# Kernel optimization log

Hardware: AMD Instinct MI355X
Metric: run time of the kernel (lower is better)

Reference implementation:

```python
import jax, jax.numpy as jnp
import numpy as np
import math

NH, NKV, D = 32, 8, 128  # heads, kv heads, head dim

def _alibi_slopes(n):
    cp2 = 2 ** math.floor(math.log2(n))
    base = 2.0 ** (-8.0 / cp2)
    slopes = base ** np.arange(1, cp2 + 1, dtype=np.float32)
    if cp2 != n:
        extra_base = 2.0 ** (-4.0 / cp2)
        extra = extra_base ** np.arange(1, 1 + 2 * (n - cp2), 2, dtype=np.float32)
        slopes = np.concatenate([slopes, extra])
    return slopes.astype(np.float32)

def setup_inputs() -> dict:
    key = jax.random.key(0)
    k1, k2, k3 = jax.random.split(key, 3)
    B, S, H = 4, 1024, 4096
    qkv_out = NH * D + 2 * NKV * D  # 6144
    return {
        "hidden_states": jax.random.normal(k1, (B, S, H), jnp.float32) * 0.02,
        "w_qkv": jax.random.normal(k2, (H, qkv_out), jnp.float32) * 0.02,
        "w_o": jax.random.normal(k3, (NH * D, H), jnp.float32) * 0.02,
    }

def reference(hidden_states, w_qkv, w_o):
    B, S, H = hidden_states.shape
    G = NH // NKV  # query groups per kv head
    scale = D ** -0.5

    qkv = hidden_states @ w_qkv  # [B,S,6144]
    q = qkv[..., : NH * D].reshape(B, S, NKV, G, D)
    k = qkv[..., NH * D : NH * D + NKV * D].reshape(B, S, NKV, D)
    v = qkv[..., NH * D + NKV * D :].reshape(B, S, NKV, D)

    scores = jnp.einsum("bqhgd,bkhd->bhgqk", q, k) * scale  # [B,NKV,G,S,S]

    slopes = jnp.asarray(_alibi_slopes(NH)).reshape(NKV, G)  # head order
    pos = jnp.arange(S)
    rel = pos[:, None] - pos[None, :]  # i - j
    sqrt_dist = jnp.sqrt(jnp.maximum(rel, 0).astype(jnp.float32))
    bias = -slopes[:, :, None, None] * sqrt_dist  # ALiBi-sqrt bias
    bias = jnp.where(rel[None, None] >= 0, bias, -jnp.inf)  # causal mask

    attn = jax.nn.softmax(scores + bias[None], axis=-1)
    out = jnp.einsum("bhgqk,bkhd->bqhgd", attn, v).reshape(B, S, NH * D)
    return out @ w_o
```

## Files before the change

kernel.cpp:

```cpp
#include <hip/hip_runtime.h>
#include <stdint.h>

typedef __attribute__((ext_vector_type(4))) float floatx4;
typedef __attribute__((ext_vector_type(8))) short short8;
typedef unsigned short ushort_t;

#define DEVI __device__ __forceinline__

constexpr int Bc   = 4;
constexpr int Sc   = 1024;
constexpr int Hc   = 4096;
constexpr int NHc  = 32;
constexpr int NKVc = 8;
constexpr int Dc   = 128;
constexpr int QKVO = 6144;
constexpr int Mc   = Bc * Sc;

DEVI ushort_t f2bf(float f) {
  union { float f; unsigned u; } x; x.f = f;
  unsigned u = x.u;
  u += 0x7fffu + ((u >> 16) & 1u);
  return (ushort_t)(u >> 16);
}

DEVI short8 cvt8(floatx4 a, floatx4 b) {
  short8 r;
  r[0] = (short)f2bf(a[0]); r[1] = (short)f2bf(a[1]);
  r[2] = (short)f2bf(a[2]); r[3] = (short)f2bf(a[3]);
  r[4] = (short)f2bf(b[0]); r[5] = (short)f2bf(b[1]);
  r[6] = (short)f2bf(b[2]); r[7] = (short)f2bf(b[3]);
  return r;
}

DEVI void load_lds16(const ushort_t* g, ushort_t* l) {
  __builtin_amdgcn_global_load_lds(
      (const __attribute__((address_space(1))) void*)g,
      (__attribute__((address_space(3))) void*)l, 16, 0, 0);
}

#define BARRIER()  asm volatile("s_barrier" ::: "memory")
#define LGKM0()    asm volatile("s_waitcnt lgkmcnt(0)" ::: "memory")
#define VMCNT(n)   asm volatile("s_waitcnt vmcnt(" #n ")" ::: "memory")

__global__ __launch_bounds__(256)
void cvt_bf16(const float* __restrict__ src, ushort_t* __restrict__ dst, int n8)
{
  const int i = blockIdx.x * 256 + threadIdx.x;
  if (i >= n8) return;
  const floatx4 f0 = *(const floatx4*)(src + (size_t)i * 8);
  const floatx4 f1 = *(const floatx4*)(src + (size_t)i * 8 + 4);
  *(short8*)(dst + (size_t)i * 8) = cvt8(f0, f1);
}

__global__ __launch_bounds__(256)
void transpose_cvt(const float* __restrict__ src, ushort_t* __restrict__ dst,
                   int R, int C)
{
  __shared__ float ts[64][67];
  const int cb = C >> 6;
  const int r0 = (blockIdx.x / cb) << 6;
  const int c0 = (blockIdx.x % cb) << 6;
  const int t  = threadIdx.x;

  const int lr = t >> 4, lc = (t & 15) << 2;
#pragma unroll
  for (int i = 0; i < 4; ++i) {
    const floatx4 v = *(const floatx4*)(src + (size_t)(r0 + lr + 16 * i) * C + c0 + lc);
#pragma unroll
    for (int j = 0; j < 4; ++j) ts[lr + 16 * i][lc + j] = v[j];
  }
  __syncthreads();

  const int c     = ((t >> 6) << 4) + ((t & 63) >> 2);
  const int chunk = t & 3;
  short8 t0, t1;
#pragma unroll
  for (int k = 0; k < 8; ++k) t0[k] = (short)f2bf(ts[chunk * 16 + k][c]);
#pragma unroll
  for (int k = 0; k < 8; ++k) t1[k] = (short)f2bf(ts[chunk * 16 + 8 + k][c]);
  ushort_t* dp = dst + (size_t)(c0 + c) * R + r0 + chunk * 16;
  *(short8*)dp       = t0;
  *(short8*)(dp + 8) = t1;
}

__global__ __launch_bounds__(256)
void v_transpose(const ushort_t* __restrict__ qkv, ushort_t* __restrict__ vt)
{
  __shared__ ushort_t ts[64][72];
  const int bid = blockIdx.x;
  const int db  = bid & 1;
  const int sb  = (bid >> 1) & 15;
  const int hkv = (bid >> 5) & 7;
  const int b   = bid >> 8;
  const int t   = threadIdx.x;

  const ushort_t* src = qkv + (size_t)(b * Sc + sb * 64) * QKVO
                        + (NHc * Dc + NKVc * Dc) + hkv * Dc + db * 64;
  const int lr = t >> 3, lc = (t & 7) * 8;
  *(short8*)&ts[lr][lc]      = *(const short8*)(src + (size_t)lr * QKVO + lc);
  *(short8*)&ts[lr + 32][lc] = *(const short8*)(src + (size_t)(lr + 32) * QKVO + lc);
  __syncthreads();

  ushort_t* dst = vt + ((size_t)(b * NKVc + hkv) * Dc + db * 64) * Sc + sb * 64;
  const int dr  = t >> 2;
  const int sc0 = (t & 3) * 16;
  short8 o0, o1;
#pragma unroll
  for (int k = 0; k < 8; ++k) o0[k] = (short)ts[sc0 + k][dr];
#pragma unroll
  for (int k = 0; k < 8; ++k) o1[k] = (short)ts[sc0 + 8 + k][dr];
  *(short8*)(dst + (size_t)dr * Sc + sc0)     = o0;
  *(short8*)(dst + (size_t)dr * Sc + sc0 + 8) = o1;
}

template<int NFRAG, bool OBF16>
__global__ __launch_bounds__(512, 2)
void gemm_nt8d(const ushort_t* __restrict__ A, const ushort_t* __restrict__ BT,
               void* __restrict__ Cp, int M, int N, int K)
{
  constexpr int BN = 64 * NFRAG;
  __shared__ __align__(16) ushort_t As[2][256 * 64];
  __shared__ __align__(16) ushort_t Bs[2][BN * 64];

  const int nb  = N / BN;
  const int nwg = (M >> 8) * nb;
  int bid = blockIdx.x;
  bid = (bid & 7) * (nwg >> 3) + (bid >> 3);
  const int bm = bid / nb, bn = bid % nb;
  const int m0 = bm << 8, n0 = bn * BN;

  const int tid  = threadIdx.x;
  const int wid  = tid >> 6, lane = tid & 63;
  const int wm   = wid >> 2, wn = wid & 3;
  const int fr   = lane & 15;
  const int g16  = (lane >> 4) << 4;
  const int rsw  = (fr & 7) << 4;
  const int l8   = lane >> 3;
  const int scol = ((lane & 7) ^ l8) << 3;

  const int sr   = (wid << 3);
  const size_t Ks = (size_t)K;
  const ushort_t* agS = A  + (size_t)(m0 + sr + l8) * K + scol;
  const ushort_t* bgS = BT + (size_t)(n0 + sr + l8) * K + scol;

  const int rowA = (wm * 128 + fr) * 128;
  const int rowB = (wn * 16 * NFRAG + fr) * 128;
  const int cb0  = g16 ^ rsw;
  const int cb1  = (64 + g16) ^ rsw;

  const floatx4 fz = {0.f, 0.f, 0.f, 0.f};
  floatx4 acc[8][NFRAG];
#pragma unroll
  for (int i = 0; i < 8; ++i)
#pragma unroll
    for (int f = 0; f < NFRAG; ++f) acc[i][f] = fz;

  auto SAq0 = [&](int s, size_t kn) {
    load_lds16(agS + kn,            &As[s][(sr +   0) * 64]);
    load_lds16(agS + 128 * Ks + kn, &As[s][(sr + 128) * 64]);
  };
  auto SAq1 = [&](int s, size_t kn) {
    load_lds16(agS +  64 * Ks + kn, &As[s][(sr +  64) * 64]);
    load_lds16(agS + 192 * Ks + kn, &As[s][(sr + 192) * 64]);
  };
  auto SB01 = [&](int s, size_t kn) {
    load_lds16(bgS + kn,            &Bs[s][(sr +   0) * 64]);
    load_lds16(bgS +  64 * Ks + kn, &Bs[s][(sr +  64) * 64]);
  };
  auto SB2 = [&](int s, size_t kn) {
    load_lds16(bgS + 128 * Ks + kn, &Bs[s][(sr + 128) * 64]);
    if constexpr (NFRAG == 4)
      load_lds16(bgS + 192 * Ks + kn, &Bs[s][(sr + 192) * 64]);
  };

  SAq0(0, 0); SAq1(0, 0); SB01(0, 0); SB2(0, 0);
  SAq0(1, 64); SB01(1, 64); SB2(1, 64);
  VMCNT(0);
  BARRIER();

#define LDA(s, i, ks) (*(const short8*)((const char*)&As[s][0] + rowA + (i) * 2048 + ((ks) ? cb1 : cb0)))
#define LDB(s, f, ks) (*(const short8*)((const char*)&Bs[s][0] + rowB + (f) * 2048 + ((ks) ? cb1 : cb0)))

  const int NI = K >> 7;
  for (int it = 0; it < NI; ++it) {
    const size_t kt0 = (size_t)it << 7;
    const size_t k1 = kt0 + 64, k2 = kt0 + 128, k3 = kt0 + 192;
    const bool st2 = (it + 1 < NI);
    const bool st3 = st2;

    short8 aR[4], bR[NFRAG][2], bS[NFRAG][2];

#define MFMA_PH(base, barr, ks)                                              \
    __builtin_amdgcn_s_setprio(1);                                          \
    _Pragma("unroll")                                                       \
    for (int i = 0; i < 4; ++i)                                             \
      _Pragma("unroll")                                                     \
      for (int f = 0; f < NFRAG; ++f)                                       \
        acc[(base) + i][f] = __builtin_amdgcn_mfma_f32_16x16x32_bf16(       \
            aR[i], barr[f][ks], acc[(base) + i][f], 0, 0, 0);               \
    __builtin_amdgcn_s_setprio(0);

#pragma unroll
    for (int i = 0; i < 4; ++i) aR[i] = LDA(0, i, 0);
#pragma unroll
    for (int f = 0; f < NFRAG; ++f) { bR[f][0] = LDB(0, f, 0); bR[f][1] = LDB(0, f, 1); }
    SAq1(1, k1);
    VMCNT(4);
    BARRIER();
    LGKM0(); __builtin_amdgcn_sched_barrier(0);
    MFMA_PH(0, bR, 0)
    BARRIER();

#pragma unroll
    for (int i = 0; i < 4; ++i) aR[i] = LDA(1, i, 0);
#pragma unroll
    for (int f = 0; f < NFRAG; ++f) { bS[f][0] = LDB(1, f, 0); bS[f][1] = LDB(1, f, 1); }
    if (st2) SB01(0, k2);
    VMCNT(4);
    BARRIER();
    LGKM0(); __builtin_amdgcn_sched_barrier(0);
    MFMA_PH(0, bS, 0)
    BARRIER();

#pragma unroll
    for (int i = 0; i < 4; ++i) aR[i] = LDA(0, 4 + i, 0);
    if (st2) SB2(0, k2);
    if constexpr (NFRAG == 4) { VMCNT(4); } else { VMCNT(3); }
    BARRIER();
    LGKM0(); __builtin_amdgcn_sched_barrier(0);
    MFMA_PH(4, bR, 0)
    BARRIER();

#pragma unroll
    for (int i = 0; i < 4; ++i) aR[i] = LDA(1, 4 + i, 0);
    if (st3) SB01(1, k3);
    BARRIER();
    LGKM0(); __builtin_amdgcn_sched_barrier(0);
    MFMA_PH(4, bS, 0)
    BARRIER();

#pragma unroll
    for (int i = 0; i < 4; ++i) aR[i] = LDA(0, i, 1);
    if (st3) SB2(1, k3);
    BARRIER();
    LGKM0(); __builtin_amdgcn_sched_barrier(0);
    MFMA_PH(0, bR, 1)
    BARRIER();

#pragma unroll
    for (int i = 0; i < 4; ++i) aR[i] = LDA(1, i, 1);
    if (st2) SAq0(0, k2);
    BARRIER();
    LGKM0(); __builtin_amdgcn_sched_barrier(0);
    MFMA_PH(0, bS, 1)
    BARRIER();

#pragma unroll
    for (int i = 0; i < 4; ++i) aR[i] = LDA(0, 4 + i, 1);
    if (st3) SAq0(1, k3);
    BARRIER();
    LGKM0(); __builtin_amdgcn_sched_barrier(0);
    MFMA_PH(4, bR, 1)
    BARRIER();

#pragma unroll
    for (int i = 0; i < 4; ++i) aR[i] = LDA(1, 4 + i, 1);
    if (st2) SAq1(0, k2);
    VMCNT(4);
    BARRIER();
    LGKM0(); __builtin_amdgcn_sched_barrier(0);
    MFMA_PH(4, bS, 1)
    BARRIER();

#undef MFMA_PH
  }
#undef LDA
#undef LDB

  const int r4 = (lane >> 4) << 2;
#pragma unroll
  for (int i = 0; i < 8; ++i) {
#pragma unroll
    for (int rr = 0; rr < 4; ++rr) {
      const size_t row = (size_t)(m0 + wm * 128 + i * 16 + r4 + rr);
#pragma unroll
      for (int f = 0; f < NFRAG; ++f) {
        const size_t col = (size_t)(n0 + wn * 16 * NFRAG + f * 16 + fr);
        if constexpr (OBF16)
          ((ushort_t*)Cp)[row * N + col] = f2bf(acc[i][f][rr]);
        else
          ((float*)Cp)[row * N + col] = acc[i][f][rr];
      }
    }
  }
}

template<int NFRAG, bool OBF16>
__global__ __launch_bounds__(512, 2)
void gemm_nt8(const ushort_t* __restrict__ A, const ushort_t* __restrict__ BT,
              void* __restrict__ Cp, int M, int N, int K)
{
  constexpr int BN = 64 * NFRAG;
  __shared__ __align__(16) ushort_t As[2][256 * 64];
  __shared__ __align__(16) ushort_t Bs[2][BN * 64];

  const int nb  = N / BN;
  const int nwg = (M >> 8) * nb;
  int bid = blockIdx.x;
  bid = (bid & 7) * (nwg >> 3) + (bid >> 3);
  const int bm = bid / nb, bn = bid % nb;
  const int m0 = bm << 8, n0 = bn * BN;

  const int tid  = threadIdx.x;
  const int wid  = tid >> 6, lane = tid & 63;
  const int wm   = wid >> 2, wn = wid & 3;
  const int fr   = lane & 15;
  const int g16  = (lane >> 4) << 4;
  const int rsw  = (fr & 7) << 4;
  const int l8   = lane >> 3;
  const int scol = ((lane & 7) ^ l8) << 3;

  const int sr   = (wid << 3);
  const size_t Ks = (size_t)K;
  const ushort_t* agS = A  + (size_t)(m0 + sr + l8) * K + scol;
  const ushort_t* bgS = BT + (size_t)(n0 + sr + l8) * K + scol;

  const int rowA = (wm * 128 + fr) * 128;
  const int rowB = (wn * 16 * NFRAG + fr) * 128;
  const int cb0  = g16 ^ rsw;
  const int cb1  = (64 + g16) ^ rsw;

  const floatx4 fz = {0.f, 0.f, 0.f, 0.f};
  floatx4 acc[8][NFRAG];
#pragma unroll
  for (int i = 0; i < 8; ++i)
#pragma unroll
    for (int f = 0; f < NFRAG; ++f) acc[i][f] = fz;

  auto STB = [&](int v, size_t kn) {
#pragma unroll
    for (int j = 0; j < NFRAG; ++j)
      load_lds16(bgS + (size_t)(64 * j) * Ks + kn, &Bs[v][(sr + 64 * j) * 64]);
  };
  auto STA = [&](int v, size_t kn) {
    load_lds16(agS + kn,            &As[v][(sr +   0) * 64]);
    load_lds16(agS + 128 * Ks + kn, &As[v][(sr + 128) * 64]);
    load_lds16(agS +  64 * Ks + kn, &As[v][(sr +  64) * 64]);
    load_lds16(agS + 192 * Ks + kn, &As[v][(sr + 192) * 64]);
  };

  STB(0, 0); STA(0, 0);
  VMCNT(2);
  BARRIER();

  const int NT = K >> 6;
  for (int kt = 0; kt < NT; ++kt) {
    const int u = kt & 1, v = u ^ 1;
    const char* Au = (const char*)&As[u][0];
    const char* Bu = (const char*)&Bs[u][0];
    const bool st  = (kt + 1 < NT);
    const size_t kn = (size_t)(kt + 1) << 6;

#define LDA(i, ks) (*(const short8*)(Au + rowA + (i) * 2048 + ((ks) ? cb1 : cb0)))
#define LDB(f, ks) (*(const short8*)(Bu + rowB + (f) * 2048 + ((ks) ? cb1 : cb0)))

    short8 aR[4], bR[NFRAG];

#pragma unroll
    for (int i = 0; i < 4; ++i) aR[i] = LDA(i, 0);
#pragma unroll
    for (int f = 0; f < NFRAG; ++f) bR[f] = LDB(f, 0);
    if (st) {
      STB(v, kn);
      if constexpr (NFRAG == 4) { VMCNT(4); } else { VMCNT(3); }
    } else { VMCNT(0); }
    BARRIER();
    LGKM0(); __builtin_amdgcn_sched_barrier(0);
    __builtin_amdgcn_s_setprio(1);
#pragma unroll
    for (int i = 0; i < 4; ++i)
#pragma unroll
      for (int f = 0; f < NFRAG; ++f)
        acc[i][f] = __builtin_amdgcn_mfma_f32_16x16x32_bf16(aR[i], bR[f], acc[i][f], 0, 0, 0);
    __builtin_amdgcn_s_setprio(0);
    BARRIER();

#pragma unroll
    for (int i = 0; i < 4; ++i) aR[i] = LDA(4 + i, 0);
    if (st) STA(v, kn);
    BARRIER();
    LGKM0(); __builtin_amdgcn_sched_barrier(0);
    __builtin_amdgcn_s_setprio(1);
#pragma unroll
    for (int i = 0; i < 4; ++i)
#pragma unroll
      for (int f = 0; f < NFRAG; ++f)
        acc[4 + i][f] = __builtin_amdgcn_mfma_f32_16x16x32_bf16(aR[i], bR[f], acc[4 + i][f], 0, 0, 0);
    __builtin_amdgcn_s_setprio(0);
    BARRIER();

#pragma unroll
    for (int i = 0; i < 4; ++i) aR[i] = LDA(4 + i, 1);
#pragma unroll
    for (int f = 0; f < NFRAG; ++f) bR[f] = LDB(f, 1);
    BARRIER();
    LGKM0(); __builtin_amdgcn_sched_barrier(0);
    __builtin_amdgcn_s_setprio(1);
#pragma unroll
    for (int i = 0; i < 4; ++i)
#pragma unroll
      for (int f = 0; f < NFRAG; ++f)
        acc[4 + i][f] = __builtin_amdgcn_mfma_f32_16x16x32_bf16(aR[i], bR[f], acc[4 + i][f], 0, 0, 0);
    __builtin_amdgcn_s_setprio(0);
    BARRIER();

#pragma unroll
    for (int i = 0; i < 4; ++i) aR[i] = LDA(i, 1);
    if (st) { VMCNT(2); }
    BARRIER();
    LGKM0(); __builtin_amdgcn_sched_barrier(0);
    __builtin_amdgcn_s_setprio(1);
#pragma unroll
    for (int i = 0; i < 4; ++i)
#pragma unroll
      for (int f = 0; f < NFRAG; ++f)
        acc[i][f] = __builtin_amdgcn_mfma_f32_16x16x32_bf16(aR[i], bR[f], acc[i][f], 0, 0, 0);
    __builtin_amdgcn_s_setprio(0);
    BARRIER();

#undef LDA
#undef LDB
  }

  const int r4 = (lane >> 4) << 2;
#pragma unroll
  for (int i = 0; i < 8; ++i) {
#pragma unroll
    for (int rr = 0; rr < 4; ++rr) {
      const size_t row = (size_t)(m0 + wm * 128 + i * 16 + r4 + rr);
#pragma unroll
      for (int f = 0; f < NFRAG; ++f) {
        const size_t col = (size_t)(n0 + wn * 16 * NFRAG + f * 16 + fr);
        if constexpr (OBF16)
          ((ushort_t*)Cp)[row * N + col] = f2bf(acc[i][f][rr]);
        else
          ((float*)Cp)[row * N + col] = acc[i][f][rr];
      }
    }
  }
}

__global__ __launch_bounds__(256, 2)
void attn_fwd(const ushort_t* __restrict__ qkv,
              const ushort_t* __restrict__ vt,
              ushort_t* __restrict__ attn)
{
  __shared__ __align__(16) ushort_t Plds[4][32 * 40];

  const int bid = blockIdx.x;
  const int x   = bid & 7;
  const int p   = bid >> 3;
  const int j   = p & 15;
  const int g   = ((p >> 4) << 3) + x;
  const int b   = g >> 3;
  const int hkv = g & 7;

  const int tid  = threadIdx.x;
  const int wid  = tid >> 6, lane = tid & 63;
  const int h    = hkv * 4 + wid;
  const int fr   = lane & 15;
  const int kk8  = (lane >> 4) << 3;
  const int q4   = (lane >> 4) << 2;
  const float slope = exp2f(-0.25f * (float)(h + 1));
  const float scale = 0.08838834764831845f;

  const ushort_t* qp  = qkv + (size_t)b * Sc * QKVO + (size_t)h * Dc;
  const ushort_t* kp  = qkv + (size_t)b * Sc * QKVO + NHc * Dc + (size_t)hkv * Dc;
  const ushort_t* vtp = vt + (size_t)(b * NKVc + hkv) * Dc * Sc;
  ushort_t* myP = &Plds[wid][0];

  const floatx4 fz = {0.f, 0.f, 0.f, 0.f};

  auto process = [&](const int qb) {
    short8 qf[2][4];
#pragma unroll
    for (int t = 0; t < 2; ++t) {
      const int qrow = qb * 32 + t * 16 + fr;
#pragma unroll
      for (int s = 0; s < 4; ++s)
        qf[t][s] = *(const short8*)(qp + (size_t)qrow * QKVO + s * 32 + kk8);
    }

    floatx4 o[2][8];
#pragma unroll
    for (int t = 0; t < 2; ++t)
#pragma unroll
      for (int jj = 0; jj < 8; ++jj) o[t][jj] = fz;
    float mrow[2][4], lrow[2][4];
#pragma unroll
    for (int t = 0; t < 2; ++t)
#pragma unroll
      for (int rr = 0; rr < 4; ++rr) { mrow[t][rr] = -1e30f; lrow[t][rr] = 0.f; }

    for (int kb = 0; kb <= qb; ++kb) {
      floatx4 s_[2][2];
      s_[0][0] = fz; s_[0][1] = fz; s_[1][0] = fz; s_[1][1] = fz;
#pragma unroll
      for (int half = 0; half < 2; ++half) {
        const int kcol = kb * 32 + half * 16 + fr;
#pragma unroll
        for (int s = 0; s < 4; ++s) {
          const short8 kf = *(const short8*)(kp + (size_t)kcol * QKVO + s * 32 + kk8);
          s_[0][half] = __builtin_amdgcn_mfma_f32_16x16x32_bf16(qf[0][s], kf, s_[0][half], 0, 0, 0);
          s_[1][half] = __builtin_amdgcn_mfma_f32_16x16x32_bf16(qf[1][s], kf, s_[1][half], 0, 0, 0);
        }
      }

      short8 vf[8];
#pragma unroll
      for (int jj = 0; jj < 8; ++jj)
        vf[jj] = *(const short8*)(vtp + (size_t)(jj * 16 + fr) * Sc + kb * 32 + kk8);

#pragma unroll
      for (int t = 0; t < 2; ++t)
#pragma unroll
        for (int rr = 0; rr < 4; ++rr) {
          const int qg  = qb * 32 + t * 16 + q4 + rr;
          const int dk0 = qg - (kb * 32 + fr);
          const int dk1 = dk0 - 16;
          s_[t][0][rr] = (dk0 >= 0)
              ? s_[t][0][rr] * scale - slope * sqrtf((float)dk0) : -1e30f;
          s_[t][1][rr] = (dk1 >= 0)
              ? s_[t][1][rr] * scale - slope * sqrtf((float)dk1) : -1e30f;
        }

      float pmv[2][4];
#pragma unroll
      for (int t = 0; t < 2; ++t)
#pragma unroll
        for (int rr = 0; rr < 4; ++rr) {
          float pm = fmaxf(s_[t][0][rr], s_[t][1][rr]);
#pragma unroll
          for (int m = 1; m < 16; m <<= 1) pm = fmaxf(pm, __shfl_xor(pm, m));
          pmv[t][rr] = pm;
        }

      int need = 0;
#pragma unroll
      for (int t = 0; t < 2; ++t)
#pragma unroll
        for (int rr = 0; rr < 4; ++rr)
          need |= (pmv[t][rr] > mrow[t][rr] + 8.f) ? 1 : 0;
      if (__any(need)) {
#pragma unroll
        for (int t = 0; t < 2; ++t)
#pragma unroll
          for (int rr = 0; rr < 4; ++rr) {
            const float mnew = fmaxf(mrow[t][rr], pmv[t][rr]);
            const float corr = __expf(mrow[t][rr] - mnew);
            lrow[t][rr] *= corr;
            mrow[t][rr] = mnew;
#pragma unroll
            for (int jj = 0; jj < 8; ++jj) o[t][jj][rr] *= corr;
          }
      }

#pragma unroll
      for (int t = 0; t < 2; ++t)
#pragma unroll
        for (int rr = 0; rr < 4; ++rr) {
          const float p0 = __expf(s_[t][0][rr] - mrow[t][rr]);
          const float p1 = __expf(s_[t][1][rr] - mrow[t][rr]);
          lrow[t][rr] += p0 + p1;
          myP[(t * 16 + q4 + rr) * 40 + fr]      = f2bf(p0);
          myP[(t * 16 + q4 + rr) * 40 + 16 + fr] = f2bf(p1);
        }
      short8 pa[2];
      pa[0] = *(const short8*)&myP[fr * 40 + kk8];
      pa[1] = *(const short8*)&myP[(16 + fr) * 40 + kk8];

#pragma unroll
      for (int jj = 0; jj < 8; ++jj) {
        o[0][jj] = __builtin_amdgcn_mfma_f32_16x16x32_bf16(pa[0], vf[jj], o[0][jj], 0, 0, 0);
        o[1][jj] = __builtin_amdgcn_mfma_f32_16x16x32_bf16(pa[1], vf[jj], o[1][jj], 0, 0, 0);
      }
    }

#pragma unroll
    for (int t = 0; t < 2; ++t)
#pragma unroll
      for (int rr = 0; rr < 4; ++rr) {
        float rs = lrow[t][rr];
#pragma unroll
        for (int m = 1; m < 16; m <<= 1) rs += __shfl_xor(rs, m);
        const float inv = 1.f / rs;
        const size_t tok = (size_t)b * Sc + qb * 32 + t * 16 + q4 + rr;
#pragma unroll
        for (int jj = 0; jj < 8; ++jj)
          attn[tok * (size_t)(NHc * Dc) + h * Dc + jj * 16 + fr] = f2bf(o[t][jj][rr] * inv);
      }
  };

  process(31 - j);
  process(j);
}

extern "C" void kernel_launch(void* const* d_in, const int* in_sizes, int n_in,
                              void* d_out, int out_size, void* d_ws, size_t ws_size,
                              hipStream_t stream)
{
  const float* hidden = (const float*)d_in[0];
  const float* w_qkv  = (const float*)d_in[1];
  const float* w_o    = (const float*)d_in[2];
  float* out = (float*)d_out;

  ushort_t* wqT   = (ushort_t*)d_ws;
  ushort_t* hidb  = wqT + (size_t)QKVO * Hc;
  ushort_t* qkvb  = hidb + (size_t)Mc * Hc;
  ushort_t* attnb = hidb;
  ushort_t* woT   = wqT;
  ushort_t* vtb   = wqT + (size_t)Mc * Hc;

  cvt_bf16<<<dim3((Mc * Hc / 8) / 256), dim3(256), 0, stream>>>(
      hidden, hidb, Mc * Hc / 8);
  transpose_cvt<<<dim3((Hc / 64) * (QKVO / 64)), dim3(256), 0, stream>>>(
      w_qkv, wqT, Hc, QKVO);
  gemm_nt8d<3, true><<<dim3((Mc / 256) * (QKVO / 192)), dim3(512), 0, stream>>>(
      hidb, wqT, qkvb, Mc, QKVO, Hc);
  v_transpose<<<dim3(1024), dim3(256), 0, stream>>>(qkvb, vtb);
  attn_fwd<<<dim3(512), dim3(256), 0, stream>>>(qkvb, vtb, attnb);
  transpose_cvt<<<dim3((Hc / 64) * (Hc / 64)), dim3(256), 0, stream>>>(
      w_o, woT, Hc, Hc);
  gemm_nt8<4, false><<<dim3((Mc / 256) * (Hc / 256)), dim3(512), 0, stream>>>(
      attnb, woT, out, Mc, Hc, Hc);
}
```

Baseline: 561.2 us.

## Restructure output GEMM prefetch into staggered split A/B loads over two k-tiles

Rewrites the output projection GEMM main loop to process two 64-wide k-tiles per iteration, splitting the global-to-LDS loads of A and B into halves issued across eight MFMA phases. B for the next tile is prefetched earlier so its loads overlap more compute, and B fragments for both k-halves are held in registers. This aims to smooth memory traffic and hide load latency, at the cost of more registers and a more intricate vmcnt/barrier schedule that must stay correct.

```diff
diff --git a/kernel.cpp b/kernel.cpp
--- a/kernel.cpp
+++ b/kernel.cpp
@@ -297,8 +297,8 @@
 
 template<int NFRAG, bool OBF16>
 __global__ __launch_bounds__(512, 2)
-void gemm_nt8(const ushort_t* __restrict__ A, const ushort_t* __restrict__ BT,
-              void* __restrict__ Cp, int M, int N, int K)
+void gemm_nt8s(const ushort_t* __restrict__ A, const ushort_t* __restrict__ BT,
+               void* __restrict__ Cp, int M, int N, int K)
 {
   constexpr int BN = 64 * NFRAG;
   __shared__ __align__(16) ushort_t As[2][256 * 64];
@@ -337,100 +337,122 @@
 #pragma unroll
     for (int f = 0; f < NFRAG; ++f) acc[i][f] = fz;
 
-  auto STB = [&](int v, size_t kn) {
-#pragma unroll
-    for (int j = 0; j < NFRAG; ++j)
-      load_lds16(bgS + (size_t)(64 * j) * Ks + kn, &Bs[v][(sr + 64 * j) * 64]);
-  };
-  auto STA = [&](int v, size_t kn) {
-    load_lds16(agS + kn,            &As[v][(sr +   0) * 64]);
-    load_lds16(agS + 128 * Ks + kn, &As[v][(sr + 128) * 64]);
-    load_lds16(agS +  64 * Ks + kn, &As[v][(sr +  64) * 64]);
-    load_lds16(agS + 192 * Ks + kn, &As[v][(sr + 192) * 64]);
-  };
-
-  STB(0, 0); STA(0, 0);
-  VMCNT(2);
+  auto SAq0 = [&](int s, size_t kn) {
+    load_lds16(agS + kn,            &As[s][(sr +   0) * 64]);
+    load_lds16(agS + 128 * Ks + kn, &As[s][(sr + 128) * 64]);
+  };
+  auto SAq1 = [&](int s, size_t kn) {
+    load_lds16(agS +  64 * Ks + kn, &As[s][(sr +  64) * 64]);
+    load_lds16(agS + 192 * Ks + kn, &As[s][(sr + 192) * 64]);
+  };
+  auto SB01 = [&](int s, size_t kn) {
+    load_lds16(bgS + kn,            &Bs[s][(sr +   0) * 64]);
+    load_lds16(bgS +  64 * Ks + kn, &Bs[s][(sr +  64) * 64]);
+  };
+  auto SB2 = [&](int s, size_t kn) {
+    load_lds16(bgS + 128 * Ks + kn, &Bs[s][(sr + 128) * 64]);
+    if constexpr (NFRAG == 4)
+      load_lds16(bgS + 192 * Ks + kn, &Bs[s][(sr + 192) * 64]);
+  };
+
+  SAq0(0, 0); SAq1(0, 0); SB01(0, 0); SB2(0, 0);
+  SB01(1, 64); SB2(1, 64);
+  VMCNT(4);
   BARRIER();
 
-  const int NT = K >> 6;
-  for (int kt = 0; kt < NT; ++kt) {
-    const int u = kt & 1, v = u ^ 1;
-    const char* Au = (const char*)&As[u][0];
-    const char* Bu = (const char*)&Bs[u][0];
-    const bool st  = (kt + 1 < NT);
-    const size_t kn = (size_t)(kt + 1) << 6;
-
-#define LDA(i, ks) (*(const short8*)(Au + rowA + (i) * 2048 + ((ks) ? cb1 : cb0)))
-#define LDB(f, ks) (*(const short8*)(Bu + rowB + (f) * 2048 + ((ks) ? cb1 : cb0)))
-
-    short8 aR[4], bR[NFRAG];
-
-#pragma unroll
-    for (int i = 0; i < 4; ++i) aR[i] = LDA(i, 0);
-#pragma unroll
-    for (int f = 0; f < NFRAG; ++f) bR[f] = LDB(f, 0);
-    if (st) {
-      STB(v, kn);
-      if constexpr (NFRAG == 4) { VMCNT(4); } else { VMCNT(3); }
-    } else { VMCNT(0); }
-    BARRIER();
-    LGKM0(); __builtin_amdgcn_sched_barrier(0);
-    __builtin_amdgcn_s_setprio(1);
-#pragma unroll
-    for (int i = 0; i < 4; ++i)
-#pragma unroll
-      for (int f = 0; f < NFRAG; ++f)
-        acc[i][f] = __builtin_amdgcn_mfma_f32_16x16x32_bf16(aR[i], bR[f], acc[i][f], 0, 0, 0);
+#define LDA(s, i, ks) (*(const short8*)((const char*)&As[s][0] + rowA + (i) * 2048 + ((ks) ? cb1 : cb0)))
+#define LDB(s, f, ks) (*(const short8*)((const char*)&Bs[s][0] + rowB + (f) * 2048 + ((ks) ? cb1 : cb0)))
+
+  const int NI = K >> 7;
+  for (int it = 0; it < NI; ++it) {
+    const size_t kt0 = (size_t)it << 7;
+    const size_t k1 = kt0 + 64, k2 = kt0 + 128, k3 = kt0 + 192;
+    const bool st = (it + 1 < NI);
+
+    short8 aR[4], bR[NFRAG][2];
+
+#define MFMA_PH(base, ks)                                                    \
+    __builtin_amdgcn_s_setprio(1);                                          \
+    _Pragma("unroll")                                                       \
+    for (int i = 0; i < 4; ++i)                                             \
+      _Pragma("unroll")                                                     \
+      for (int f = 0; f < NFRAG; ++f)                                       \
+        acc[(base) + i][f] = __builtin_amdgcn_mfma_f32_16x16x32_bf16(       \
+            aR[i], bR[f][ks], acc[(base) + i][f], 0, 0, 0);                 \
     __builtin_amdgcn_s_setprio(0);
-    BARRIER();
-
-#pragma unroll
-    for (int i = 0; i < 4; ++i) aR[i] = LDA(4 + i, 0);
-    if (st) STA(v, kn);
-    BARRIER();
-    LGKM0(); __builtin_amdgcn_sched_barrier(0);
-    __builtin_amdgcn_s_setprio(1);
-#pragma unroll
-    for (int i = 0; i < 4; ++i)
-#pragma unroll
-      for (int f = 0; f < NFRAG; ++f)
-        acc[4 + i][f] = __builtin_amdgcn_mfma_f32_16x16x32_bf16(aR[i], bR[f], acc[4 + i][f], 0, 0, 0);
-    __builtin_amdgcn_s_setprio(0);
-    BARRIER();
-
-#pragma unroll
-    for (int i = 0; i < 4; ++i) aR[i] = LDA(4 + i, 1);
-#pragma unroll
-    for (int f = 0; f < NFRAG; ++f) bR[f] = LDB(f, 1);
-    BARRIER();
-    LGKM0(); __builtin_amdgcn_sched_barrier(0);
-    __builtin_amdgcn_s_setprio(1);
-#pragma unroll
-    for (int i = 0; i < 4; ++i)
-#pragma unroll
-      for (int f = 0; f < NFRAG; ++f)
-        acc[4 + i][f] = __builtin_amdgcn_mfma_f32_16x16x32_bf16(aR[i], bR[f], acc[4 + i][f], 0, 0, 0);
-    __builtin_amdgcn_s_setprio(0);
-    BARRIER();
-
-#pragma unroll
-    for (int i = 0; i < 4; ++i) aR[i] = LDA(i, 1);
-    if (st) { VMCNT(2); }
-    BARRIER();
-    LGKM0(); __builtin_amdgcn_sched_barrier(0);
-    __builtin_amdgcn_s_setprio(1);
-#pragma unroll
-    for (int i = 0; i < 4; ++i)
-#pragma unroll
-      for (int f = 0; f < NFRAG; ++f)
-        acc[i][f] = __builtin_amdgcn_mfma_f32_16x16x32_bf16(aR[i], bR[f], acc[i][f], 0, 0, 0);
-    __builtin_amdgcn_s_setprio(0);
-    BARRIER();
-
+
+#pragma unroll
+    for (int i = 0; i < 4; ++i) aR[i] = LDA(0, i, 0);
+#pragma unroll
+    for (int f = 0; f < NFRAG; ++f) { bR[f][0] = LDB(0, f, 0); bR[f][1] = LDB(0, f, 1); }
+    SAq0(1, k1);
+    BARRIER();
+    LGKM0(); __builtin_amdgcn_sched_barrier(0);
+    MFMA_PH(0, 0)
+    BARRIER();
+
+#pragma unroll
+    for (int i = 0; i < 4; ++i) aR[i] = LDA(0, 4 + i, 0);
+    SAq1(1, k1);
+    BARRIER();
+    LGKM0(); __builtin_amdgcn_sched_barrier(0);
+    MFMA_PH(4, 0)
+    BARRIER();
+
+#pragma unroll
+    for (int i = 0; i < 4; ++i) aR[i] = LDA(0, i, 1);
+    if (st) SB01(0, k2);
+    BARRIER();
+    LGKM0(); __builtin_amdgcn_sched_barrier(0);
+    MFMA_PH(0, 1)
+    BARRIER();
+
+#pragma unroll
+    for (int i = 0; i < 4; ++i) aR[i] = LDA(0, 4 + i, 1);
+    if (st) { SB2(0, k2); VMCNT(4); } else { VMCNT(0); }
+    BARRIER();
+    LGKM0(); __builtin_amdgcn_sched_barrier(0);
+    MFMA_PH(4, 1)
+    BARRIER();
+
+#pragma unroll
+    for (int i = 0; i < 4; ++i) aR[i] = LDA(1, i, 0);
+#pragma unroll
+    for (int f = 0; f < NFRAG; ++f) { bR[f][0] = LDB(1, f, 0); bR[f][1] = LDB(1, f, 1); }
+    if (st) SAq0(0, k2);
+    BARRIER();
+    LGKM0(); __builtin_amdgcn_sched_barrier(0);
+    MFMA_PH(0, 0)
+    BARRIER();
+
+#pragma unroll
+    for (int i = 0; i < 4; ++i) aR[i] = LDA(1, 4 + i, 0);
+    if (st) SAq1(0, k2);
+    BARRIER();
+    LGKM0(); __builtin_amdgcn_sched_barrier(0);
+    MFMA_PH(4, 0)
+    BARRIER();
+
+#pragma unroll
+    for (int i = 0; i < 4; ++i) aR[i] = LDA(1, i, 1);
+    if (st) SB01(1, k3);
+    BARRIER();
+    LGKM0(); __builtin_amdgcn_sched_barrier(0);
+    MFMA_PH(0, 1)
+    BARRIER();
+
+#pragma unroll
+    for (int i = 0; i < 4; ++i) aR[i] = LDA(1, 4 + i, 1);
+    if (st) { SB2(1, k3); VMCNT(4); } else { VMCNT(0); }
+    BARRIER();
+    LGKM0(); __builtin_amdgcn_sched_barrier(0);
+    MFMA_PH(4, 1)
+    BARRIER();
+
+#undef MFMA_PH
+  }
 #undef LDA
 #undef LDB
-  }
 
   const int r4 = (lane >> 4) << 2;
 #pragma unroll
@@ -631,6 +653,6 @@
   attn_fwd<<<dim3(512), dim3(256), 0, stream>>>(qkvb, vtb, attnb);
   transpose_cvt<<<dim3((Hc / 64) * (Hc / 64)), dim3(256), 0, stream>>>(
       w_o, woT, Hc, Hc);
-  gemm_nt8<4, false><<<dim3((Mc / 256) * (Hc / 256)), dim3(512), 0, stream>>>(
+  gemm_nt8s<4, false><<<dim3((Mc / 256) * (Hc / 256)), dim3(512), 0, stream>>>(
       attnb, woT, out, Mc, Hc, Hc);
 }
```

New measurement: 559.7 us (median of 2 runs). No clear change (-0.3%).
